# Kernel tuning notes

Hardware: AMD Instinct MI355X
Metric: run time of the kernel (lower is better)

The kernel has to match this reference:

```python
import jax, jax.numpy as jnp
import numpy as np

N = 50000      # nodes
K = 15         # k_max candidate neighbors per node
D = 128        # node_dim
H = 64         # hidden_dim
K_MIN = 2.0
K_MAX = 15.0
TAU = 0.5      # edge_tau
LAM = 1.0      # selector_lambda


def setup_inputs() -> dict:
    key = jax.random.key(0)
    ks = jax.random.split(key, 16)
    x = jax.random.normal(ks[0], (N, D), dtype=jnp.float32)
    src = jax.random.randint(ks[1], (N * K,), 0, N)
    dst = jnp.repeat(jnp.arange(N), K)  # edges grouped by dst, as the module requires
    edge_index = jnp.stack([src, dst]).astype(jnp.int64)
    edge_dist = jax.random.uniform(ks[2], (N * K,), dtype=jnp.float32)

    def lin(k, fin, fout):
        return jax.random.normal(k, (fin, fout), dtype=jnp.float32) / np.sqrt(fin)

    EIN = 2 * D + 1  # edge MLP input: [x_dst, x_src, dist]
    return {
        "x": x, "edge_index": edge_index, "edge_dist": edge_dist,
        "ew1": lin(ks[3], EIN, H), "eb1": jnp.zeros((H,), jnp.float32),
        "ew2": lin(ks[4], H, H),   "eb2": jnp.zeros((H,), jnp.float32),
        "ew3": lin(ks[5], H, 1),   "eb3": jnp.zeros((1,), jnp.float32),
        "dw1": lin(ks[6], D + 1, H), "db1": jnp.zeros((H,), jnp.float32),
        "dw2": lin(ks[7], H, H),     "db2": jnp.zeros((H,), jnp.float32),
        "dw3": lin(ks[8], H, 1),     "db3": jnp.zeros((1,), jnp.float32),
    }


def reference(x, edge_index, edge_dist, ew1, eb1, ew2, eb2, ew3, eb3,
              dw1, db1, dw2, db2, dw3, db3):
    src_mat = edge_index[0].reshape(N, K)              # (N, K)
    x_src = x[src_mat]                                 # gather: (N, K, D)
    x_dst = jnp.broadcast_to(x[:, None, :], (N, K, D))
    edge_feat = jnp.concatenate([x_dst, x_src, edge_dist.reshape(N, K, 1)], axis=-1)

    # edge MLP -> logits (eval mode: no gumbel-logistic noise)
    h = jax.nn.relu(edge_feat @ ew1 + eb1)
    h = jax.nn.relu(h @ ew2 + eb2)
    edge_logits = (h @ ew3 + eb3)[..., 0]              # (N, K)
    edge_energy = jax.nn.sigmoid(edge_logits / TAU)

    # degree MLP -> continuous k per node
    degree_hint = edge_energy.sum(axis=1, keepdims=True)
    g = jax.nn.relu(jnp.concatenate([x, degree_hint], axis=1) @ dw1 + db1)
    g = jax.nn.relu(g @ dw2 + db2)
    k_raw = (g @ dw3 + db3)[:, 0]
    k_cont = K_MIN + (K_MAX - K_MIN) * jax.nn.sigmoid(k_raw)  # (N,)

    # per-node descending sort + straight-through top-k gate
    perm = jnp.argsort(-edge_energy, axis=1)
    energy_sorted = jnp.take_along_axis(edge_energy, perm, axis=1)
    ranks = jnp.arange(1, K + 1, dtype=x.dtype)[None, :]
    gate_soft = jax.nn.sigmoid((k_cont[:, None] - ranks) / LAM)
    k_int = jnp.clip(jnp.round(k_cont), K_MIN, K_MAX)
    gate_hard = (ranks <= k_int[:, None]).astype(gate_soft.dtype)
    gate = gate_soft + jax.lax.stop_gradient(gate_hard - gate_soft)

    gated_sorted = energy_sorted * gate
    inv_perm = jnp.argsort(perm, axis=1)               # undo the sort
    edge_gate = jnp.take_along_axis(gate, inv_perm, axis=1)
    edge_weight = jnp.take_along_axis(gated_sorted, inv_perm, axis=1)

    denom = jnp.maximum(edge_weight.sum(axis=1, keepdims=True), 1e-12)
    edge_weight = edge_weight / denom
    return (edge_weight.reshape(-1), edge_gate.reshape(-1),
            edge_energy.reshape(-1), k_cont)
```

## Files before the change

### kernel.cpp

```cpp
#include <hip/hip_runtime.h>
#include <cmath>

#define NN 50000
#define KK 15
#define DD 128
#define HH 64
#define NKE (NN * KK)

__global__ __launch_bounds__(256) void kP(const float* __restrict__ x,
                                          const float* __restrict__ ew1,
                                          const float* __restrict__ dw1,
                                          float* __restrict__ ws) {
    int lane = threadIdx.x & 63;
    int wv = __builtin_amdgcn_readfirstlane((int)(threadIdx.x >> 6));
    int r0 = blockIdx.x * 32 + wv * 8;
    if (r0 >= NN) return;

    const float* W0 = ew1;
    const float* W1 = ew1 + DD * HH;
    const float* W2 = dw1;
    const float* xw = x + (size_t)r0 * DD;

    float a0[8], a1[8], a2[8];
#pragma unroll
    for (int r = 0; r < 8; ++r) { a0[r] = 0.f; a1[r] = 0.f; a2[r] = 0.f; }

#pragma unroll 1
    for (int i4 = 0; i4 < DD / 4; ++i4) {
        float w00 = W0[(i4 * 4 + 0) * HH + lane];
        float w01 = W0[(i4 * 4 + 1) * HH + lane];
        float w02 = W0[(i4 * 4 + 2) * HH + lane];
        float w03 = W0[(i4 * 4 + 3) * HH + lane];
        float w10 = W1[(i4 * 4 + 0) * HH + lane];
        float w11 = W1[(i4 * 4 + 1) * HH + lane];
        float w12 = W1[(i4 * 4 + 2) * HH + lane];
        float w13 = W1[(i4 * 4 + 3) * HH + lane];
        float w20 = W2[(i4 * 4 + 0) * HH + lane];
        float w21 = W2[(i4 * 4 + 1) * HH + lane];
        float w22 = W2[(i4 * 4 + 2) * HH + lane];
        float w23 = W2[(i4 * 4 + 3) * HH + lane];
#pragma unroll
        for (int r = 0; r < 8; ++r) {
            float4 xv = *(const float4*)(xw + r * DD + i4 * 4);
            a0[r] = fmaf(xv.x, w00, a0[r]);
            a0[r] = fmaf(xv.y, w01, a0[r]);
            a0[r] = fmaf(xv.z, w02, a0[r]);
            a0[r] = fmaf(xv.w, w03, a0[r]);
            a1[r] = fmaf(xv.x, w10, a1[r]);
            a1[r] = fmaf(xv.y, w11, a1[r]);
            a1[r] = fmaf(xv.z, w12, a1[r]);
            a1[r] = fmaf(xv.w, w13, a1[r]);
            a2[r] = fmaf(xv.x, w20, a2[r]);
            a2[r] = fmaf(xv.y, w21, a2[r]);
            a2[r] = fmaf(xv.z, w22, a2[r]);
            a2[r] = fmaf(xv.w, w23, a2[r]);
        }
    }
    float* o0 = ws + (size_t)r0 * HH + lane;
    float* o1 = ws + (size_t)NN * HH + (size_t)r0 * HH + lane;
    float* o2 = ws + 2 * (size_t)NN * HH + (size_t)r0 * HH + lane;
#pragma unroll
    for (int r = 0; r < 8; ++r) {
        o0[r * HH] = a0[r];
        o1[r * HH] = a1[r];
        o2[r * HH] = a2[r];
    }
}

__global__ __launch_bounds__(128, 4) void kE(const int* __restrict__ srcIdx,
                                             const float* __restrict__ dist,
                                             const float* __restrict__ ws,
                                             const float* __restrict__ ew1,
                                             const float* __restrict__ eb1,
                                             const float* __restrict__ ew2,
                                             const float* __restrict__ eb2,
                                             const float* __restrict__ ew3,
                                             const float* __restrict__ eb3,
                                             float* __restrict__ energy_out) {
    int e = blockIdx.x * 128 + threadIdx.x;
    if (e >= NKE) return;
    int s = srcIdx[e];
    int d = e / KK;
    float dd = dist[e];
    const float* A = ws + (size_t)d * HH;
    const float* B = ws + (size_t)NN * HH + (size_t)s * HH;
    const float* w1l = ew1 + 2 * DD * HH;

    float acc[HH];
#pragma unroll
    for (int j = 0; j < HH; ++j) acc[j] = 0.f;

    float4 a4 = *(const float4*)A;
    float4 b4 = *(const float4*)B;
#pragma unroll 1
    for (int i4 = 0; i4 < HH / 4; ++i4) {
        float4 a = a4, b = b4;
        int nx = (i4 + 1 < HH / 4) ? (i4 + 1) : i4;
        a4 = *(const float4*)(A + nx * 4);
        b4 = *(const float4*)(B + nx * 4);
        float h[4];
        h[0] = fmaxf(a.x + b.x + dd * w1l[i4 * 4 + 0] + eb1[i4 * 4 + 0], 0.f);
        h[1] = fmaxf(a.y + b.y + dd * w1l[i4 * 4 + 1] + eb1[i4 * 4 + 1], 0.f);
        h[2] = fmaxf(a.z + b.z + dd * w1l[i4 * 4 + 2] + eb1[i4 * 4 + 2], 0.f);
        h[3] = fmaxf(a.w + b.w + dd * w1l[i4 * 4 + 3] + eb1[i4 * 4 + 3], 0.f);
#pragma unroll
        for (int k = 0; k < 4; ++k) {
            const float* wr = ew2 + (i4 * 4 + k) * HH;
#pragma unroll
            for (int j4 = 0; j4 < 16; ++j4) {
                float4 w = *(const float4*)(wr + j4 * 4);
                acc[j4 * 4 + 0] = fmaf(h[k], w.x, acc[j4 * 4 + 0]);
                acc[j4 * 4 + 1] = fmaf(h[k], w.y, acc[j4 * 4 + 1]);
                acc[j4 * 4 + 2] = fmaf(h[k], w.z, acc[j4 * 4 + 2]);
                acc[j4 * 4 + 3] = fmaf(h[k], w.w, acc[j4 * 4 + 3]);
            }
        }
    }
    float lg = eb3[0];
#pragma unroll
    for (int j = 0; j < HH; ++j)
        lg = fmaf(fmaxf(acc[j] + eb2[j], 0.f), ew3[j], lg);
    energy_out[e] = 1.f / (1.f + expf(-2.f * lg));
}

__global__ __launch_bounds__(128, 4) void kF(const float* __restrict__ ws,
                                             const float* __restrict__ dw1,
                                             const float* __restrict__ db1,
                                             const float* __restrict__ dw2,
                                             const float* __restrict__ db2,
                                             const float* __restrict__ dw3,
                                             const float* __restrict__ db3,
                                             float* __restrict__ out) {
    int n = blockIdx.x * 128 + threadIdx.x;
    if (n >= NN) return;
    const float* energy = out + 2 * (size_t)NKE;

    float ev[KK];
    float dh = 0.f;
#pragma unroll
    for (int j = 0; j < KK; ++j) {
        ev[j] = energy[(size_t)n * KK + j];
        dh += ev[j];
    }

    const float* XC = ws + 2 * (size_t)NN * HH + (size_t)n * HH;
    const float* w1l = dw1 + DD * HH;

    float acc[HH];
#pragma unroll
    for (int j = 0; j < HH; ++j) acc[j] = 0.f;

    float4 c4 = *(const float4*)XC;
#pragma unroll 1
    for (int i4 = 0; i4 < HH / 4; ++i4) {
        float4 c = c4;
        int nx = (i4 + 1 < HH / 4) ? (i4 + 1) : i4;
        c4 = *(const float4*)(XC + nx * 4);
        float cv[4] = {c.x, c.y, c.z, c.w};
#pragma unroll
        for (int m = 0; m < 4; ++m) {
            int k = i4 * 4 + m;
            float g = fmaxf(cv[m] + dh * w1l[k] + db1[k], 0.f);
            const float* wr = dw2 + k * HH;
#pragma unroll
            for (int j4 = 0; j4 < 16; ++j4) {
                float4 w = *(const float4*)(wr + j4 * 4);
                acc[j4 * 4 + 0] = fmaf(g, w.x, acc[j4 * 4 + 0]);
                acc[j4 * 4 + 1] = fmaf(g, w.y, acc[j4 * 4 + 1]);
                acc[j4 * 4 + 2] = fmaf(g, w.z, acc[j4 * 4 + 2]);
                acc[j4 * 4 + 3] = fmaf(g, w.w, acc[j4 * 4 + 3]);
            }
        }
    }
    float kraw = db3[0];
#pragma unroll
    for (int j = 0; j < HH; ++j)
        kraw = fmaf(fmaxf(acc[j] + db2[j], 0.f), dw3[j], kraw);

    float kcont = 2.f + 13.f / (1.f + expf(-kraw));
    out[3 * (size_t)NKE + n] = kcont;

    float se[16];
    int si[16];
#pragma unroll
    for (int j = 0; j < KK; ++j) { se[j] = ev[j]; si[j] = j; }
    se[15] = -1.f; si[15] = 15;

#pragma unroll
    for (int p = 1; p < 16; p <<= 1) {
#pragma unroll
        for (int k = p; k >= 1; k >>= 1) {
#pragma unroll
            for (int j = k & (p - 1); j + k < 16; j += 2 * k) {
#pragma unroll
                for (int i = 0; i < k; ++i) {
                    int a = i + j, b = i + j + k;
                    if (b < 16 && (a / (2 * p)) == (b / (2 * p))) {
                        bool sw = (se[b] > se[a]) ||
                                  (se[b] == se[a] && si[b] < si[a]);
                        float ea = sw ? se[b] : se[a];
                        float eb = sw ? se[a] : se[b];
                        int ia = sw ? si[b] : si[a];
                        int ib = sw ? si[a] : si[b];
                        se[a] = ea; se[b] = eb; si[a] = ia; si[b] = ib;
                    }
                }
            }
        }
    }

    float kint = rintf(kcont);
    kint = fminf(fmaxf(kint, 2.f), 15.f);

    float wsrt[KK];
    float denom = 0.f;
#pragma unroll
    for (int r = 0; r < KK; ++r) {
        float sel = ((float)(r + 1) <= kint) ? 1.f : 0.f;
        float wvv = se[r] * sel;
        wsrt[r] = wvv;
        denom += wvv;
    }
    denom = fmaxf(denom, 1e-12f);

#pragma unroll
    for (int r = 0; r < KK; ++r) {
        float sel = ((float)(r + 1) <= kint) ? 1.f : 0.f;
        int j0 = si[r];
        out[(size_t)NKE + (size_t)n * KK + j0] = sel;
        out[(size_t)n * KK + j0] = wsrt[r] / denom;
    }
}

extern "C" void kernel_launch(void* const* d_in, const int* in_sizes, int n_in,
                              void* d_out, int out_size, void* d_ws, size_t ws_size,
                              hipStream_t stream) {
    const float* x   = (const float*)d_in[0];
    const int*   ei  = (const int*)d_in[1];
    const float* ed  = (const float*)d_in[2];
    const float* ew1 = (const float*)d_in[3];
    const float* eb1 = (const float*)d_in[4];
    const float* ew2 = (const float*)d_in[5];
    const float* eb2 = (const float*)d_in[6];
    const float* ew3 = (const float*)d_in[7];
    const float* eb3 = (const float*)d_in[8];
    const float* dw1 = (const float*)d_in[9];
    const float* db1 = (const float*)d_in[10];
    const float* dw2 = (const float*)d_in[11];
    const float* db2 = (const float*)d_in[12];
    const float* dw3 = (const float*)d_in[13];
    const float* db3 = (const float*)d_in[14];
    float* out = (float*)d_out;
    float* ws  = (float*)d_ws;

    hipLaunchKernelGGL(kP, dim3((NN + 31) / 32), dim3(256), 0, stream,
                       x, ew1, dw1, ws);
    hipLaunchKernelGGL(kE, dim3((NKE + 127) / 128), dim3(128), 0, stream,
                       ei, ed, ws, ew1, eb1, ew2, eb2, ew3, eb3,
                       out + 2 * (size_t)NKE);
    hipLaunchKernelGGL(kF, dim3((NN + 127) / 128), dim3(128), 0, stream,
                       ws, dw1, db1, dw2, db2, dw3, db3, out);
}
```

Baseline: 269.3 us.

## Tune launch bounds, deepen src prefetch in kE, chunk kF accumulators

```diff
diff --git a/kernel.cpp b/kernel.cpp
--- a/kernel.cpp
+++ b/kernel.cpp
@@ -7,12 +7,12 @@
 #define HH 64
 #define NKE (NN * KK)
 
-__global__ __launch_bounds__(256) void kP(const float* __restrict__ x,
-                                          const float* __restrict__ ew1,
-                                          const float* __restrict__ dw1,
-                                          float* __restrict__ ws) {
+__global__ __launch_bounds__(256, 4) void kP(const float* __restrict__ x,
+                                             const float* __restrict__ ew1,
+                                             const float* __restrict__ dw1,
+                                             float* __restrict__ ws) {
     int lane = threadIdx.x & 63;
-    int wv = __builtin_amdgcn_readfirstlane((int)(threadIdx.x >> 6));
+    int wv = threadIdx.x >> 6;
     int r0 = blockIdx.x * 32 + wv * 8;
     if (r0 >= NN) return;
 
@@ -91,13 +91,16 @@
     for (int j = 0; j < HH; ++j) acc[j] = 0.f;
 
     float4 a4 = *(const float4*)A;
-    float4 b4 = *(const float4*)B;
+    float4 bp0 = *(const float4*)B;
+    float4 bp1 = *(const float4*)(B + 4);
 #pragma unroll 1
     for (int i4 = 0; i4 < HH / 4; ++i4) {
-        float4 a = a4, b = b4;
-        int nx = (i4 + 1 < HH / 4) ? (i4 + 1) : i4;
-        a4 = *(const float4*)(A + nx * 4);
-        b4 = *(const float4*)(B + nx * 4);
+        float4 a = a4, b = bp0;
+        int n1 = (i4 + 1 < 16) ? (i4 + 1) : 15;
+        int n2 = (i4 + 2 < 16) ? (i4 + 2) : 15;
+        a4 = *(const float4*)(A + n1 * 4);
+        bp0 = bp1;
+        bp1 = *(const float4*)(B + n2 * 4);
         float h[4];
         h[0] = fmaxf(a.x + b.x + dd * w1l[i4 * 4 + 0] + eb1[i4 * 4 + 0], 0.f);
         h[1] = fmaxf(a.y + b.y + dd * w1l[i4 * 4 + 1] + eb1[i4 * 4 + 1], 0.f);
@@ -123,7 +126,7 @@
     energy_out[e] = 1.f / (1.f + expf(-2.f * lg));
 }
 
-__global__ __launch_bounds__(128, 4) void kF(const float* __restrict__ ws,
+__global__ __launch_bounds__(256, 4) void kF(const float* __restrict__ ws,
                                              const float* __restrict__ dw1,
                                              const float* __restrict__ db1,
                                              const float* __restrict__ dw2,
@@ -131,7 +134,7 @@
                                              const float* __restrict__ dw3,
                                              const float* __restrict__ db3,
                                              float* __restrict__ out) {
-    int n = blockIdx.x * 128 + threadIdx.x;
+    int n = blockIdx.x * 256 + threadIdx.x;
     if (n >= NN) return;
     const float* energy = out + 2 * (size_t)NKE;
 
@@ -145,37 +148,40 @@
 
     const float* XC = ws + 2 * (size_t)NN * HH + (size_t)n * HH;
     const float* w1l = dw1 + DD * HH;
-
-    float acc[HH];
-#pragma unroll
-    for (int j = 0; j < HH; ++j) acc[j] = 0.f;
-
-    float4 c4 = *(const float4*)XC;
-#pragma unroll 1
-    for (int i4 = 0; i4 < HH / 4; ++i4) {
-        float4 c = c4;
-        int nx = (i4 + 1 < HH / 4) ? (i4 + 1) : i4;
-        c4 = *(const float4*)(XC + nx * 4);
-        float cv[4] = {c.x, c.y, c.z, c.w};
-#pragma unroll
-        for (int m = 0; m < 4; ++m) {
-            int k = i4 * 4 + m;
-            float g = fmaxf(cv[m] + dh * w1l[k] + db1[k], 0.f);
-            const float* wr = dw2 + k * HH;
-#pragma unroll
-            for (int j4 = 0; j4 < 16; ++j4) {
-                float4 w = *(const float4*)(wr + j4 * 4);
-                acc[j4 * 4 + 0] = fmaf(g, w.x, acc[j4 * 4 + 0]);
-                acc[j4 * 4 + 1] = fmaf(g, w.y, acc[j4 * 4 + 1]);
-                acc[j4 * 4 + 2] = fmaf(g, w.z, acc[j4 * 4 + 2]);
-                acc[j4 * 4 + 3] = fmaf(g, w.w, acc[j4 * 4 + 3]);
+    float kraw = db3[0];
+
+#pragma unroll 1
+    for (int c = 0; c < 4; ++c) {
+        float acc[16];
+#pragma unroll
+        for (int t = 0; t < 16; ++t) acc[t] = 0.f;
+#pragma unroll 1
+        for (int k4 = 0; k4 < 16; ++k4) {
+            float4 cx = *(const float4*)(XC + k4 * 4);
+            float cv[4] = {cx.x, cx.y, cx.z, cx.w};
+#pragma unroll
+            for (int m = 0; m < 4; ++m) {
+                int k = k4 * 4 + m;
+                float g = fmaxf(cv[m] + dh * w1l[k] + db1[k], 0.f);
+                const float* wr = dw2 + k * HH + c * 16;
+                float4 wA = *(const float4*)(wr + 0);
+                float4 wB = *(const float4*)(wr + 4);
+                float4 wC = *(const float4*)(wr + 8);
+                float4 wD = *(const float4*)(wr + 12);
+                acc[0]  = fmaf(g, wA.x, acc[0]);  acc[1]  = fmaf(g, wA.y, acc[1]);
+                acc[2]  = fmaf(g, wA.z, acc[2]);  acc[3]  = fmaf(g, wA.w, acc[3]);
+                acc[4]  = fmaf(g, wB.x, acc[4]);  acc[5]  = fmaf(g, wB.y, acc[5]);
+                acc[6]  = fmaf(g, wB.z, acc[6]);  acc[7]  = fmaf(g, wB.w, acc[7]);
+                acc[8]  = fmaf(g, wC.x, acc[8]);  acc[9]  = fmaf(g, wC.y, acc[9]);
+                acc[10] = fmaf(g, wC.z, acc[10]); acc[11] = fmaf(g, wC.w, acc[11]);
+                acc[12] = fmaf(g, wD.x, acc[12]); acc[13] = fmaf(g, wD.y, acc[13]);
+                acc[14] = fmaf(g, wD.z, acc[14]); acc[15] = fmaf(g, wD.w, acc[15]);
             }
         }
-    }
-    float kraw = db3[0];
-#pragma unroll
-    for (int j = 0; j < HH; ++j)
-        kraw = fmaf(fmaxf(acc[j] + db2[j], 0.f), dw3[j], kraw);
+#pragma unroll
+        for (int t = 0; t < 16; ++t)
+            kraw = fmaf(fmaxf(acc[t] + db2[c * 16 + t], 0.f), dw3[c * 16 + t], kraw);
+    }
 
     float kcont = 2.f + 13.f / (1.f + expf(-kraw));
     out[3 * (size_t)NKE + n] = kcont;
@@ -258,6 +264,6 @@
     hipLaunchKernelGGL(kE, dim3((NKE + 127) / 128), dim3(128), 0, stream,
                        ei, ed, ws, ew1, eb1, ew2, eb2, ew3, eb3,
                        out + 2 * (size_t)NKE);
-    hipLaunchKernelGGL(kF, dim3((NN + 127) / 128), dim3(128), 0, stream,
+    hipLaunchKernelGGL(kF, dim3((NN + 255) / 256), dim3(256), 0, stream,
                        ws, dw1, db1, dw2, db2, dw3, db3, out);
 }
```

After: 316.8 us. +17.7%, slower.
